# Kernel optimization log

Hardware: AMD Instinct MI355X
Metric: run time of the kernel (lower is better)

The kernel has to match this reference:

```python
import jax, jax.numpy as jnp
import numpy as np

V, E, H2, T = 50000, 256, 512, 16  # vocab, embed, hidden_dim, tagset
H = H2 // 2                        # per-direction hidden
START, STOP = 14, 15
NEG = -10000.0


def setup_inputs() -> dict:
    key = jax.random.key(0)
    ks = jax.random.split(key, 13)
    s = 0.08
    tokens = jax.random.randint(ks[0], (32, 512), 0, V)
    embed_table = jax.random.normal(ks[1], (V, E), jnp.float32)
    Wi_f = jax.random.normal(ks[2], (4 * H, E), jnp.float32) * s
    Wh_f = jax.random.normal(ks[3], (4 * H, H), jnp.float32) * s
    bi_f = jnp.zeros((4 * H,), jnp.float32)
    bh_f = jnp.zeros((4 * H,), jnp.float32)
    Wi_b = jax.random.normal(ks[4], (4 * H, E), jnp.float32) * s
    Wh_b = jax.random.normal(ks[5], (4 * H, H), jnp.float32) * s
    bi_b = jnp.zeros((4 * H,), jnp.float32)
    bh_b = jnp.zeros((4 * H,), jnp.float32)
    Wt = jax.random.normal(ks[6], (T, H2), jnp.float32) * s
    bt = jnp.zeros((T,), jnp.float32)
    trans = jax.random.normal(ks[7], (T, T), jnp.float32)
    trans = trans.at[START, :].set(NEG).at[:, STOP].set(NEG)
    return {"tokens": tokens, "embed_table": embed_table,
            "Wi_f": Wi_f, "Wh_f": Wh_f, "bi_f": bi_f, "bh_f": bh_f,
            "Wi_b": Wi_b, "Wh_b": Wh_b, "bi_b": bi_b, "bh_b": bh_b,
            "Wt": Wt, "bt": bt, "transitions": trans}


def _lstm_dir(x, Wi, Wh, bi, bh, reverse=False):
    # x: [S, B, E] -> h seq [S, B, H], PyTorch gate order i,f,g,o
    S, B, _ = x.shape
    xs = x[::-1] if reverse else x
    pre = jnp.einsum('sbe,ge->sbg', xs, Wi) + bi + bh  # precompute input GEMM

    def step(carry, z_t):
        h, c = carry
        z = z_t + h @ Wh.T  # [B, 4H]
        i, f, g, o = jnp.split(z, 4, axis=-1)
        c = jax.nn.sigmoid(f) * c + jax.nn.sigmoid(i) * jnp.tanh(g)
        h = jax.nn.sigmoid(o) * jnp.tanh(c)
        return (h, c), h

    h0 = jnp.zeros((B, H), x.dtype)
    _, hs = jax.lax.scan(step, (h0, h0), pre)
    return hs[::-1] if reverse else hs


def reference(tokens, embed_table, Wi_f, Wh_f, bi_f, bh_f,
              Wi_b, Wh_b, bi_b, bh_b, Wt, bt, transitions):
    x = embed_table[tokens]                # [B, S, E]
    x = jnp.transpose(x, (1, 0, 2))        # [S, B, E] seq-first like nn.LSTM
    hf = _lstm_dir(x, Wi_f, Wh_f, bi_f, bh_f, reverse=False)
    hb = _lstm_dir(x, Wi_b, Wh_b, bi_b, bh_b, reverse=True)
    feats = jnp.concatenate([hf, hb], axis=-1)           # [S, B, 2H]
    emissions = jnp.einsum('sbh,th->sbt', feats, Wt) + bt  # [S, B, T]

    B = tokens.shape[0]
    alpha0 = jnp.full((B, T), NEG, jnp.float32).at[:, START].set(0.0)

    def crf_step(alpha, emit_t):
        # alpha: [B, T_prev]; transitions[next, prev]; emit_t: [B, T_next]
        scores = alpha[:, None, :] + transitions[None, :, :] + emit_t[:, :, None]
        return jax.nn.logsumexp(scores, axis=2), None

    alpha, _ = jax.lax.scan(crf_step, alpha0, emissions)
    log_Z = jax.nn.logsumexp(alpha + transitions[STOP][None, :], axis=1)  # [B]
    return log_Z
```

## Files before the change

### kernel.cpp

```cpp
#include <hip/hip_runtime.h>
#include <hip/hip_bf16.h>
#include <stdint.h>

typedef __attribute__((ext_vector_type(4))) float f32x4;
typedef __attribute__((ext_vector_type(8))) short bf16x8;

#define WS_XBF   0u
#define WS_WIR   8388608u
#define WS_BIAS  9437184u
#define WS_PRE   9445376u
#define WS_HALL  76554240u
#define WS_CTL   93364224u
#define WS_EMIS  93368320u
#define WS_CHK   94416896u
#define WS_FLG   WS_CHK

__device__ __forceinline__ unsigned short f2bf(float x) {
    union { float f; unsigned int u; } v; v.f = x;
    return (unsigned short)((v.u + 0x7FFFu + ((v.u >> 16) & 1u)) >> 16);
}
__device__ __forceinline__ float bf2f(unsigned short b) {
    union { float f; unsigned int u; } v; v.u = ((unsigned int)b) << 16; return v.f;
}
__device__ __forceinline__ unsigned int pack2(float a, float b) {
    return (unsigned int)f2bf(a) | ((unsigned int)f2bf(b) << 16);
}
__device__ __forceinline__ float sigf(float x)  { return 1.0f / (1.0f + __expf(-x)); }
__device__ __forceinline__ float tanhf_(float x){ return 1.0f - 2.0f / (__expf(2.0f * x) + 1.0f); }

__device__ __forceinline__ void lds_barrier() {
    asm volatile("s_waitcnt lgkmcnt(0)" ::: "memory");
    __builtin_amdgcn_s_barrier();
    __builtin_amdgcn_sched_barrier(0);
}

__global__ __launch_bounds__(256) void k_prep(
    const int* __restrict__ tokens, const float* __restrict__ embed,
    const float* __restrict__ Wi_f, const float* __restrict__ Wi_b,
    const float* __restrict__ bi_f, const float* __restrict__ bh_f,
    const float* __restrict__ bi_b, const float* __restrict__ bh_b,
    char* __restrict__ ws)
{
    int blk = blockIdx.x, tid = threadIdx.x;
    unsigned short* xbf  = (unsigned short*)(ws + WS_XBF);
    unsigned short* wir  = (unsigned short*)(ws + WS_WIR);
    float* biasr         = (float*)(ws + WS_BIAS);
    if (blk < 2048) {
        int rr = tid >> 5, cc = tid & 31;
        int r = blk * 8 + rr;
        int s = r >> 5, b = r & 31;
        int tok = tokens[b * 512 + s];
        int k = cc * 8;
        const float* src = embed + (size_t)tok * 256 + k;
        float4 a = *(const float4*)src;
        float4 c = *(const float4*)(src + 4);
        uint4 o; o.x = pack2(a.x, a.y); o.y = pack2(a.z, a.w);
        o.z = pack2(c.x, c.y); o.w = pack2(c.z, c.w);
        *(uint4*)(xbf + (size_t)r * 256 + k) = o;
    } else if (blk < 2304) {
        int rr = tid >> 5, cc = tid & 31;
        int rowp = (blk - 2048) * 8 + rr;
        int dir = rowp >> 10, q = rowp & 1023;
        int j = q >> 8, rs = q & 255;
        int g = rs >> 6, hl = rs & 63;
        int srow = g * 256 + j * 64 + hl;
        const float* W = dir ? Wi_b : Wi_f;
        int k = cc * 8;
        const float* src = W + (size_t)srow * 256 + k;
        float4 a = *(const float4*)src;
        float4 c = *(const float4*)(src + 4);
        uint4 o; o.x = pack2(a.x, a.y); o.y = pack2(a.z, a.w);
        o.z = pack2(c.x, c.y); o.w = pack2(c.z, c.w);
        *(uint4*)(wir + (size_t)rowp * 256 + k) = o;
        if (cc == 0)
            biasr[rowp] = dir ? (bi_b[srow] + bh_b[srow]) : (bi_f[srow] + bh_f[srow]);
    } else {
        if (blk == 2304 && tid < 16)
            ((unsigned int*)(ws + WS_CTL))[tid] = 0u;
        if (blk == 2305) {
            unsigned int* flg = (unsigned int*)(ws + WS_FLG);
            for (int u = tid; u < 2 * 513 * 4 * 32; u += 256) flg[u] = 0u;
        }
        size_t g = (size_t)(blk - 2304) * 256 + tid;
        uint4* hall4 = (uint4*)(ws + WS_HALL);
        const unsigned int NF = 0xFFFFFFFFu;
        for (size_t u = g; u < 1050624u; u += 65536u) {
            size_t slot = (u >> 10) % 513u;
            uint4 val;
            if (slot == 0) { val.x = 0u; val.y = 0u; val.z = 0u; val.w = 0u; }
            else           { val.x = NF; val.y = NF; val.z = NF; val.w = NF; }
            hall4[u] = val;
        }
    }
}

__global__ __launch_bounds__(256) void k_pregemm(char* __restrict__ ws)
{
    __shared__ unsigned short Asb[128 * 136];
    __shared__ unsigned short Bsb[64 * 136];
    const unsigned short* xbf = (const unsigned short*)(ws + WS_XBF);
    const unsigned short* wir = (const unsigned short*)(ws + WS_WIR);
    const float* biasr        = (const float*)(ws + WS_BIAS);
    unsigned short* pre       = (unsigned short*)(ws + WS_PRE);
    int blk = blockIdx.x, tid = threadIdx.x;
    int mb = blk >> 5, nb = blk & 31;
    int Mbase = mb * 128, Nbase = nb * 64;
    int w = tid >> 6, l = tid & 63, col = l & 15, quad = l >> 4;
    f32x4 acc[4][2];
    #pragma unroll
    for (int a = 0; a < 4; ++a)
        #pragma unroll
        for (int b = 0; b < 2; ++b) acc[a][b] = (f32x4){0.f, 0.f, 0.f, 0.f};

    for (int kh = 0; kh < 2; ++kh) {
        __syncthreads();
        #pragma unroll
        for (int i = 0; i < 8; ++i) {
            int c = tid + i * 256;
            int row = c >> 4, c16 = c & 15;
            uint4 v = *(const uint4*)(xbf + ((size_t)(Mbase + row) * 256 + kh * 128 + c16 * 8));
            *(uint4*)(Asb + row * 136 + c16 * 8) = v;
        }
        #pragma unroll
        for (int i = 0; i < 4; ++i) {
            int c = tid + i * 256;
            int row = c >> 4, c16 = c & 15;
            uint4 v = *(const uint4*)(wir + ((size_t)(Nbase + row) * 256 + kh * 128 + c16 * 8));
            *(uint4*)(Bsb + row * 136 + c16 * 8) = v;
        }
        __syncthreads();
        int mhalf = w >> 1, nh = w & 1;
        #pragma unroll
        for (int kt = 0; kt < 4; ++kt) {
            bf16x8 bfr[2];
            #pragma unroll
            for (int nn = 0; nn < 2; ++nn)
                bfr[nn] = *(const bf16x8*)(Bsb + (16 * (nh * 2 + nn) + col) * 136 + kt * 32 + quad * 8);
            #pragma unroll
            for (int mm = 0; mm < 4; ++mm) {
                bf16x8 afr = *(const bf16x8*)(Asb + (16 * (mhalf * 4 + mm) + col) * 136 + kt * 32 + quad * 8);
                #pragma unroll
                for (int nn = 0; nn < 2; ++nn)
                    acc[mm][nn] = __builtin_amdgcn_mfma_f32_16x16x32_bf16(afr, bfr[nn], acc[mm][nn], 0, 0, 0);
            }
        }
    }
    #pragma unroll
    for (int mm = 0; mm < 4; ++mm) {
        int m_t = (w >> 1) * 4 + mm;
        int s = (Mbase >> 5) + (m_t >> 1);
        int bhalf = m_t & 1;
        #pragma unroll
        for (int nn = 0; nn < 2; ++nn) {
            int ncol = Nbase + 16 * ((w & 1) * 2 + nn) + col;
            int dir = ncol >> 10, j = (ncol >> 8) & 3, r = ncol & 255;
            int g = r >> 6, hl16 = (r >> 4) & 3;
            int tidp = (bhalf * 4 + hl16) * 64 + l;
            float bv = biasr[ncol];
            f32x4 a = acc[mm][nn];
            uint2 o;
            o.x = pack2(a[0] + bv, a[1] + bv);
            o.y = pack2(a[2] + bv, a[3] + bv);
            size_t off = (((size_t)(dir * 512 + s) * 4 + j) * 512 + tidp) * 16 + g * 4;
            *(uint2*)(pre + off) = o;
        }
    }
}

__global__ __launch_bounds__(512, 2) void k_rec(
    const float* __restrict__ Wh_f, const float* __restrict__ Wh_b, char* __restrict__ ws)
{
    __shared__ unsigned short hbuf[32 * 264];
    __shared__ char stpad[71680];
    __shared__ int sRole;
    __shared__ int goCnt;
    int tid = threadIdx.x;

    if (tid == 0) {
        ((volatile char*)stpad)[0] = 0;
        goCnt = 0;
        int xcd;
        asm volatile("s_getreg_b32 %0, hwreg(HW_REG_XCC_ID)" : "=s"(xcd));
        xcd &= 7;
        unsigned int* ctl = (unsigned int*)(ws + WS_CTL);
        unsigned int slot = __hip_atomic_fetch_add(&ctl[xcd], 1u,
                              __ATOMIC_RELAXED, __HIP_MEMORY_SCOPE_AGENT);
        int role = -1;
        if (slot < 8u) {
            if (slot == 7u) {
                unsigned int expv = 0u;
                __hip_atomic_compare_exchange_strong(&ctl[8], &expv, (unsigned int)(xcd + 1),
                    __ATOMIC_RELAXED, __ATOMIC_RELAXED, __HIP_MEMORY_SCOPE_AGENT);
            }
            unsigned int ts; long gc = 0;
            do {
                ts = __hip_atomic_fetch_add(&ctl[8], 0u,
                        __ATOMIC_RELAXED, __HIP_MEMORY_SCOPE_AGENT);
            } while (ts == 0u && ++gc < (1L << 26));
            if (ts == (unsigned int)(xcd + 1)) role = (int)slot;
        }
        sRole = role;
    }
    __syncthreads();
    int role = sRole;
    if (role < 0) return;
    int dir = role >> 2, j = role & 3;

    int w = tid >> 6, l = tid & 63, col = l & 15, quad = l >> 4;
    int m = w >> 2, hl16 = w & 3;
    const float* Wh = dir ? Wh_b : Wh_f;
    const unsigned short* pre = (const unsigned short*)(ws + WS_PRE);
    unsigned short* hall      = (unsigned short*)(ws + WS_HALL);
    unsigned int* flags       = (unsigned int*)(ws + WS_FLG);

    bf16x8 wf[4][8];
    #pragma unroll
    for (int g = 0; g < 4; ++g) {
        int grow = g * 256 + j * 64 + hl16 * 16 + col;
        #pragma unroll
        for (int kt = 0; kt < 8; ++kt) {
            const float* src = Wh + (size_t)grow * 256 + kt * 32 + quad * 8;
            float4 x0 = *(const float4*)src;
            float4 x1 = *(const float4*)(src + 4);
            bf16x8 f;
            f[0] = (short)f2bf(x0.x); f[1] = (short)f2bf(x0.y);
            f[2] = (short)f2bf(x0.z); f[3] = (short)f2bf(x0.w);
            f[4] = (short)f2bf(x1.x); f[5] = (short)f2bf(x1.y);
            f[6] = (short)f2bf(x1.z); f[7] = (short)f2bf(x1.w);
            wf[g][kt] = f;
        }
    }
    __syncthreads();

    float cst[4] = {0.f, 0.f, 0.f, 0.f};
    size_t hbase_u = (size_t)dir * 513 * 8192;
    int row0 = tid >> 6, c8 = tid & 63;
    int jr = (tid < 3) ? (tid + (tid >= j ? 1 : 0)) : -1;

    uint4 pn0, pn1;
    {
        int s0 = dir ? 511 : 0;
        const uint4* pp = (const uint4*)(pre + ((((size_t)(dir * 512 + s0)) * 4 + j) * 512 + tid) * 16);
        pn0 = pp[0]; pn1 = pp[1];
    }

    for (int st = 0; st < 512; ++st) {
        uint4 p0 = pn0, p1 = pn1;

        if (st > 0) {
            if (jr >= 0) {
                unsigned int* fl = flags + ((size_t)((dir * 513 + st) * 4 + jr)) * 32;
                int rnd = 0;
                for (;;) {
                    unsigned int expv = 0u;
                    __hip_atomic_compare_exchange_strong(fl, &expv, 0u,
                        __ATOMIC_RELAXED, __ATOMIC_RELAXED, __HIP_MEMORY_SCOPE_WORKGROUP);
                    if (expv != 0u) break;
                    if (++rnd > (1 << 18)) break;
                }
                __hip_atomic_fetch_add(&goCnt, 1, __ATOMIC_RELAXED, __HIP_MEMORY_SCOPE_WORKGROUP);
            }
            int target = 3 * st;
            long sg = 0;
            while (__hip_atomic_load(&goCnt, __ATOMIC_RELAXED, __HIP_MEMORY_SCOPE_WORKGROUP) < target) {
                if (++sg > (1L << 21)) break;
            }
            asm volatile("" ::: "memory");
        }

        const unsigned short* hsl = hall + hbase_u + (size_t)st * 8192;
        unsigned long long v[4];
        #pragma unroll
        for (int i = 0; i < 4; ++i)
            v[i] = *(const unsigned long long*)(hsl + (size_t)(tid + i * 512) * 4);
        #pragma unroll
        for (int i = 0; i < 4; ++i)
            *(unsigned long long*)(hbuf + (row0 + i * 8) * 264 + c8 * 4) = v[i];
        lds_barrier();

        f32x4 acc[4];
        #pragma unroll
        for (int g = 0; g < 4; ++g) acc[g] = (f32x4){0.f, 0.f, 0.f, 0.f};
        #pragma unroll
        for (int kt = 0; kt < 8; ++kt) {
            bf16x8 af = *(const bf16x8*)(hbuf + (m * 16 + col) * 264 + kt * 32 + quad * 8);
            #pragma unroll
            for (int g = 0; g < 4; ++g)
                acc[g] = __builtin_amdgcn_mfma_f32_16x16x32_bf16(af, wf[g][kt], acc[g], 0, 0, 0);
        }
        unsigned int pw[8] = {p0.x, p0.y, p0.z, p0.w, p1.x, p1.y, p1.z, p1.w};
        float z[4][4];
        #pragma unroll
        for (int g = 0; g < 4; ++g) {
            #pragma unroll
            for (int r2 = 0; r2 < 2; ++r2) {
                unsigned int u = pw[g * 2 + r2];
                z[g][r2 * 2]     = acc[g][r2 * 2]     + bf2f((unsigned short)(u & 0xffff));
                z[g][r2 * 2 + 1] = acc[g][r2 * 2 + 1] + bf2f((unsigned short)(u >> 16));
            }
        }
        unsigned short hb16[4];
        #pragma unroll
        for (int r = 0; r < 4; ++r) {
            float ci = sigf(z[1][r]) * cst[r] + sigf(z[0][r]) * tanhf_(z[2][r]);
            cst[r] = ci;
            hb16[r] = f2bf(sigf(z[3][r]) * tanhf_(ci));
        }
        size_t dstb = hbase_u + (size_t)(st + 1) * 8192
                    + (size_t)(m * 16 + quad * 4) * 256 + j * 64 + hl16 * 16 + col;
        #pragma unroll
        for (int r = 0; r < 4; ++r)
            *(hall + dstb + (size_t)r * 256) = hb16[r];
        asm volatile("s_waitcnt vmcnt(0)" ::: "memory");
        __builtin_amdgcn_s_barrier();
        __builtin_amdgcn_sched_barrier(0);
        if (tid == 0)
            (void)__hip_atomic_exchange(flags + ((size_t)((dir * 513 + st + 1) * 4 + j)) * 32, 1u,
                                        __ATOMIC_RELAXED, __HIP_MEMORY_SCOPE_WORKGROUP);
        {
            int stn = (st < 511) ? st + 1 : st;
            int sn = dir ? (511 - stn) : stn;
            const uint4* pp = (const uint4*)(pre + ((((size_t)(dir * 512 + sn)) * 4 + j) * 512 + tid) * 16);
            pn0 = pp[0]; pn1 = pp[1];
        }
    }
}

__global__ __launch_bounds__(256) void k_emis(
    const float* __restrict__ Wt, const float* __restrict__ bt, char* __restrict__ ws)
{
    __shared__ float WtL[16 * 528];
    __shared__ unsigned short hrow[16 * 536];
    __shared__ float btL[16];
    int blk = blockIdx.x, tid = threadIdx.x;
    int sbb = blk * 16;
    int s = sbb >> 5, bbase = sbb & 31;
    const unsigned short* hall = (const unsigned short*)(ws + WS_HALL);
    float* emis = (float*)(ws + WS_EMIS);
    #pragma unroll
    for (int i = 0; i < 8; ++i) {
        int c = tid + i * 256;
        int trow = c >> 7, c128 = c & 127;
        float4 v = *(const float4*)(Wt + (size_t)trow * 512 + c128 * 4);
        *(float4*)(WtL + trow * 528 + c128 * 4) = v;
    }
    #pragma unroll
    for (int i = 0; i < 4; ++i) {
        int c = tid + i * 256;
        int row = c >> 6, c6 = c & 63, half = c6 >> 5, c16 = c6 & 31;
        size_t base = half == 0 ? (size_t)(s + 1) * 8192 : ((size_t)513 + (512 - s)) * 8192;
        uint4 v = *(const uint4*)(hall + base + (size_t)(bbase + row) * 256 + c16 * 8);
        *(uint4*)(hrow + row * 536 + half * 256 + c16 * 8) = v;
    }
    if (tid < 16) btL[tid] = bt[tid];
    __syncthreads();
    int t = tid >> 4, i = tid & 15;
    float acc = btL[t];
    const float* wrow = WtL + t * 528;
    const unsigned short* hr = hrow + i * 536;
    #pragma unroll 8
    for (int k = 0; k < 512; k += 4) {
        uint2 hu = *(const uint2*)(hr + k);
        float4 wv = *(const float4*)(wrow + k);
        acc += bf2f((unsigned short)(hu.x & 0xffff)) * wv.x
             + bf2f((unsigned short)(hu.x >> 16))    * wv.y
             + bf2f((unsigned short)(hu.y & 0xffff)) * wv.z
             + bf2f((unsigned short)(hu.y >> 16))    * wv.w;
    }
    emis[((size_t)(bbase + i) * 512 + s) * 16 + t] = acc;
}

__global__ __launch_bounds__(256) void k_crfc(const float* __restrict__ trans, char* __restrict__ ws)
{
    __shared__ float trL[16 * 17];
    __shared__ float est[16 * 16];
    __shared__ float Pb[2][16 * 17];
    int blk = blockIdx.x, tid = threadIdx.x;
    int b = blk >> 5, c = blk & 31;
    int t = tid >> 4, p = tid & 15;
    const float* emis = (const float*)(ws + WS_EMIS);
    float* chk = (float*)(ws + WS_CHK);
    trL[t * 17 + p] = trans[t * 16 + p];
    est[t * 16 + p] = emis[((size_t)b * 512 + c * 16 + t) * 16 + p];
    __syncthreads();
    float tr[16];
    #pragma unroll
    for (int q = 0; q < 16; ++q) tr[q] = trL[t * 17 + q];
    float out = trL[t * 17 + p] + est[0 * 16 + t];
    Pb[0][t * 17 + p] = out;
    __syncthreads();
    int cur = 0;
    for (int si = 1; si < 16; ++si) {
        float v[16]; float mx = -3.0e38f;
        #pragma unroll
        for (int q = 0; q < 16; ++q) { v[q] = tr[q] + Pb[cur][q * 17 + p]; mx = fmaxf(mx, v[q]); }
        float ss = 0.f;
        #pragma unroll
        for (int q = 0; q < 16; ++q) ss += __expf(v[q] - mx);
        out = est[si * 16 + t] + mx + __logf(ss);
        Pb[1 - cur][t * 17 + p] = out;
        __syncthreads();
        cur = 1 - cur;
    }
    chk[(size_t)(b * 32 + c) * 256 + t * 16 + p] = out;
}

__global__ __launch_bounds__(256) void k_crff(
    const float* __restrict__ trans, char* __restrict__ ws, float* __restrict__ out)
{
    __shared__ float Cst[16 * 17];
    __shared__ float Pb[2][16 * 17];
    __shared__ float af[16];
    int b = blockIdx.x, tid = threadIdx.x;
    int t = tid >> 4, p = tid & 15;
    const float* chk = (const float*)(ws + WS_CHK);
    Pb[0][t * 17 + p] = chk[(size_t)(b * 32) * 256 + t * 16 + p];
    __syncthreads();
    int cur = 0;
    for (int ci = 1; ci < 32; ++ci) {
        Cst[t * 17 + p] = chk[(size_t)(b * 32 + ci) * 256 + t * 16 + p];
        __syncthreads();
        float v[16]; float mx = -3.0e38f;
        #pragma unroll
        for (int q = 0; q < 16; ++q) { v[q] = Cst[t * 17 + q] + Pb[cur][q * 17 + p]; mx = fmaxf(mx, v[q]); }
        float ss = 0.f;
        #pragma unroll
        for (int q = 0; q < 16; ++q) ss += __expf(v[q] - mx);
        float outv = mx + __logf(ss);
        Pb[1 - cur][t * 17 + p] = outv;
        __syncthreads();
        cur = 1 - cur;
    }
    float vfin = Pb[cur][t * 17 + p] + ((p == 14) ? 0.0f : -10000.0f);
    Cst[t * 17 + p] = vfin;
    __syncthreads();
    if (tid < 16) {
        float mx = -3.0e38f;
        for (int q = 0; q < 16; ++q) mx = fmaxf(mx, Cst[tid * 17 + q]);
        float ss = 0.f;
        for (int q = 0; q < 16; ++q) ss += __expf(Cst[tid * 17 + q] - mx);
        af[tid] = mx + __logf(ss) + trans[15 * 16 + tid];
    }
    __syncthreads();
    if (tid == 0) {
        float mx = -3.0e38f;
        for (int q = 0; q < 16; ++q) mx = fmaxf(mx, af[q]);
        float ss = 0.f;
        for (int q = 0; q < 16; ++q) ss += __expf(af[q] - mx);
        out[b] = mx + __logf(ss);
    }
}

extern "C" void kernel_launch(void* const* d_in, const int* in_sizes, int n_in,
                              void* d_out, int out_size, void* d_ws, size_t ws_size,
                              hipStream_t stream)
{
    const int*   tokens = (const int*)d_in[0];
    const float* embed  = (const float*)d_in[1];
    const float* Wi_f   = (const float*)d_in[2];
    const float* Wh_f   = (const float*)d_in[3];
    const float* bi_f   = (const float*)d_in[4];
    const float* bh_f   = (const float*)d_in[5];
    const float* Wi_b   = (const float*)d_in[6];
    const float* Wh_b   = (const float*)d_in[7];
    const float* bi_b   = (const float*)d_in[8];
    const float* bh_b   = (const float*)d_in[9];
    const float* Wt     = (const float*)d_in[10];
    const float* bt     = (const float*)d_in[11];
    const float* trans  = (const float*)d_in[12];
    char* ws = (char*)d_ws;
    float* out = (float*)d_out;

    hipLaunchKernelGGL(k_prep, dim3(2560), dim3(256), 0, stream,
                       tokens, embed, Wi_f, Wi_b, bi_f, bh_f, bi_b, bh_b, ws);
    hipLaunchKernelGGL(k_pregemm, dim3(4096), dim3(256), 0, stream, ws);
    hipLaunchKernelGGL(k_rec, dim3(128), dim3(512), 0, stream, Wh_f, Wh_b, ws);
    hipLaunchKernelGGL(k_emis, dim3(1024), dim3(256), 0, stream, Wt, bt, ws);
    hipLaunchKernelGGL(k_crfc, dim3(1024), dim3(256), 0, stream, trans, ws);
    hipLaunchKernelGGL(k_crff, dim3(32), dim3(256), 0, stream, trans, ws, out);
}
```

Measured before the change: 1.724 ms.

## Repartition LSTM recurrence by batch half and hidden half with local LDS reuse

The recurrent kernel changes from 4 blocks per direction each owning a 64-unit hidden slice over all 32 batch rows to 2x2 blocks per direction each owning 16 batch rows and 128 hidden units. Each block keeps its own half of h in double-buffered LDS and starts the MFMAs on that local half before waiting on the single peer's flag, then loads only the peer half from global memory. This cuts each step's wait from three producers to one and overlaps part of the recurrent GEMM with that wait. The hall layout, flag indexing, init and emission loader are reworked to match, and the spin timeouts are shortened, which could cause silent early exits if a peer stalls.

```diff
diff --git a/kernel.cpp b/kernel.cpp
--- a/kernel.cpp
+++ b/kernel.cpp
@@ -79,18 +79,13 @@
             ((unsigned int*)(ws + WS_CTL))[tid] = 0u;
         if (blk == 2305) {
             unsigned int* flg = (unsigned int*)(ws + WS_FLG);
-            for (int u = tid; u < 2 * 513 * 4 * 32; u += 256) flg[u] = 0u;
+            for (int u = tid; u < 4 * 513 * 2 * 32; u += 256) flg[u] = 0u;
         }
         size_t g = (size_t)(blk - 2304) * 256 + tid;
         uint4* hall4 = (uint4*)(ws + WS_HALL);
-        const unsigned int NF = 0xFFFFFFFFu;
-        for (size_t u = g; u < 1050624u; u += 65536u) {
-            size_t slot = (u >> 10) % 513u;
-            uint4 val;
-            if (slot == 0) { val.x = 0u; val.y = 0u; val.z = 0u; val.w = 0u; }
-            else           { val.x = NF; val.y = NF; val.z = NF; val.w = NF; }
-            hall4[u] = val;
-        }
+        uint4 z; z.x = 0u; z.y = 0u; z.z = 0u; z.w = 0u;
+        for (size_t u = g; u < 1050624u; u += 65536u)
+            hall4[u] = z;
     }
 }
 
@@ -170,15 +165,15 @@
 __global__ __launch_bounds__(512, 2) void k_rec(
     const float* __restrict__ Wh_f, const float* __restrict__ Wh_b, char* __restrict__ ws)
 {
-    __shared__ unsigned short hbuf[32 * 264];
+    __shared__ unsigned short hbuf[2 * 16 * 264];
     __shared__ char stpad[71680];
     __shared__ int sRole;
-    __shared__ int goCnt;
+    __shared__ int go;
     int tid = threadIdx.x;
 
     if (tid == 0) {
         ((volatile char*)stpad)[0] = 0;
-        goCnt = 0;
+        go = 0;
         int xcd;
         asm volatile("s_getreg_b32 %0, hwreg(HW_REG_XCC_ID)" : "=s"(xcd));
         xcd &= 7;
@@ -204,10 +199,9 @@
     __syncthreads();
     int role = sRole;
     if (role < 0) return;
-    int dir = role >> 2, j = role & 3;
+    int dir = role >> 2, b2 = (role >> 1) & 1, uh = role & 1;
 
     int w = tid >> 6, l = tid & 63, col = l & 15, quad = l >> 4;
-    int m = w >> 2, hl16 = w & 3;
     const float* Wh = dir ? Wh_b : Wh_f;
     const unsigned short* pre = (const unsigned short*)(ws + WS_PRE);
     unsigned short* hall      = (unsigned short*)(ws + WS_HALL);
@@ -216,7 +210,7 @@
     bf16x8 wf[4][8];
     #pragma unroll
     for (int g = 0; g < 4; ++g) {
-        int grow = g * 256 + j * 64 + hl16 * 16 + col;
+        int grow = g * 256 + uh * 128 + w * 16 + col;
         #pragma unroll
         for (int kt = 0; kt < 8; ++kt) {
             const float* src = Wh + (size_t)grow * 256 + kt * 32 + quad * 8;
@@ -230,64 +224,81 @@
             wf[g][kt] = f;
         }
     }
+    for (int u = tid; u < 4224; u += 512) ((unsigned int*)hbuf)[u] = 0;
     __syncthreads();
 
     float cst[4] = {0.f, 0.f, 0.f, 0.f};
-    size_t hbase_u = (size_t)dir * 513 * 8192;
-    int row0 = tid >> 6, c8 = tid & 63;
-    int jr = (tid < 3) ? (tid + (tid >= j ? 1 : 0)) : -1;
+    int jpre = uh * 2 + (w >> 2);
+    int tidp = (b2 * 4 + (w & 3)) * 64 + l;
+    size_t rb = (size_t)(dir * 2 + b2) * 513;
+    int rrow = l >> 2, cpart = l & 3;
 
     uint4 pn0, pn1;
     {
         int s0 = dir ? 511 : 0;
-        const uint4* pp = (const uint4*)(pre + ((((size_t)(dir * 512 + s0)) * 4 + j) * 512 + tid) * 16);
+        const uint4* pp = (const uint4*)(pre + ((((size_t)(dir * 512 + s0)) * 4 + jpre) * 512 + tidp) * 16);
         pn0 = pp[0]; pn1 = pp[1];
     }
 
     for (int st = 0; st < 512; ++st) {
+        int cur = st & 1;
+        unsigned short* hb_cur = hbuf + cur * 4224;
+        unsigned short* hb_nxt = hbuf + (cur ^ 1) * 4224;
         uint4 p0 = pn0, p1 = pn1;
+        {
+            int stn = (st < 511) ? st + 1 : st;
+            int sn = dir ? (511 - stn) : stn;
+            const uint4* pp = (const uint4*)(pre + ((((size_t)(dir * 512 + sn)) * 4 + jpre) * 512 + tidp) * 16);
+            pn0 = pp[0]; pn1 = pp[1];
+        }
+
+        f32x4 acc[4];
+        #pragma unroll
+        for (int g = 0; g < 4; ++g) acc[g] = (f32x4){0.f, 0.f, 0.f, 0.f};
+
+        #pragma unroll
+        for (int k2 = 0; k2 < 4; ++k2) {
+            int kt = uh * 4 + k2;
+            bf16x8 af = *(const bf16x8*)(hb_cur + col * 264 + kt * 32 + quad * 8);
+            #pragma unroll
+            for (int g = 0; g < 4; ++g)
+                acc[g] = __builtin_amdgcn_mfma_f32_16x16x32_bf16(af, wf[g][kt], acc[g], 0, 0, 0);
+        }
 
         if (st > 0) {
-            if (jr >= 0) {
-                unsigned int* fl = flags + ((size_t)((dir * 513 + st) * 4 + jr)) * 32;
+            if (tid == 0) {
+                unsigned int* fl = flags + ((rb + st) * 2 + (uh ^ 1)) * 32;
                 int rnd = 0;
                 for (;;) {
                     unsigned int expv = 0u;
                     __hip_atomic_compare_exchange_strong(fl, &expv, 0u,
                         __ATOMIC_RELAXED, __ATOMIC_RELAXED, __HIP_MEMORY_SCOPE_WORKGROUP);
                     if (expv != 0u) break;
-                    if (++rnd > (1 << 18)) break;
+                    if (++rnd > (1 << 16)) break;
                 }
-                __hip_atomic_fetch_add(&goCnt, 1, __ATOMIC_RELAXED, __HIP_MEMORY_SCOPE_WORKGROUP);
+                __hip_atomic_store(&go, st, __ATOMIC_RELAXED, __HIP_MEMORY_SCOPE_WORKGROUP);
             }
-            int target = 3 * st;
             long sg = 0;
-            while (__hip_atomic_load(&goCnt, __ATOMIC_RELAXED, __HIP_MEMORY_SCOPE_WORKGROUP) < target) {
-                if (++sg > (1L << 21)) break;
+            while (__hip_atomic_load(&go, __ATOMIC_RELAXED, __HIP_MEMORY_SCOPE_WORKGROUP) < st) {
+                if (++sg > (1L << 20)) break;
             }
             asm volatile("" ::: "memory");
-        }
-
-        const unsigned short* hsl = hall + hbase_u + (size_t)st * 8192;
-        unsigned long long v[4];
-        #pragma unroll
-        for (int i = 0; i < 4; ++i)
-            v[i] = *(const unsigned long long*)(hsl + (size_t)(tid + i * 512) * 4);
-        #pragma unroll
-        for (int i = 0; i < 4; ++i)
-            *(unsigned long long*)(hbuf + (row0 + i * 8) * 264 + c8 * 4) = v[i];
+            size_t srcb = (rb + st) * 4096 + (size_t)(uh ^ 1) * 2048 + (size_t)tid * 4;
+            unsigned long long pv = *(const unsigned long long*)(hall + srcb);
+            int prow = tid >> 5, ploc = (tid * 4) & 127;
+            *(unsigned long long*)(hb_cur + prow * 264 + (uh ^ 1) * 128 + ploc) = pv;
+        }
         lds_barrier();
 
-        f32x4 acc[4];
-        #pragma unroll
-        for (int g = 0; g < 4; ++g) acc[g] = (f32x4){0.f, 0.f, 0.f, 0.f};
-        #pragma unroll
-        for (int kt = 0; kt < 8; ++kt) {
-            bf16x8 af = *(const bf16x8*)(hbuf + (m * 16 + col) * 264 + kt * 32 + quad * 8);
+        #pragma unroll
+        for (int k2 = 0; k2 < 4; ++k2) {
+            int kt = (uh ^ 1) * 4 + k2;
+            bf16x8 af = *(const bf16x8*)(hb_cur + col * 264 + kt * 32 + quad * 8);
             #pragma unroll
             for (int g = 0; g < 4; ++g)
                 acc[g] = __builtin_amdgcn_mfma_f32_16x16x32_bf16(af, wf[g][kt], acc[g], 0, 0, 0);
         }
+
         unsigned int pw[8] = {p0.x, p0.y, p0.z, p0.w, p1.x, p1.y, p1.z, p1.w};
         float z[4][4];
         #pragma unroll
@@ -306,23 +317,21 @@
             cst[r] = ci;
             hb16[r] = f2bf(sigf(z[3][r]) * tanhf_(ci));
         }
-        size_t dstb = hbase_u + (size_t)(st + 1) * 8192
-                    + (size_t)(m * 16 + quad * 4) * 256 + j * 64 + hl16 * 16 + col;
         #pragma unroll
         for (int r = 0; r < 4; ++r)
-            *(hall + dstb + (size_t)r * 256) = hb16[r];
-        asm volatile("s_waitcnt vmcnt(0)" ::: "memory");
+            hb_nxt[(quad * 4 + r) * 264 + uh * 128 + w * 16 + col] = hb16[r];
+        asm volatile("s_waitcnt lgkmcnt(0)" ::: "memory");
+        __builtin_amdgcn_sched_barrier(0);
+        unsigned long long hv = *(const unsigned long long*)
+            (hb_nxt + rrow * 264 + uh * 128 + w * 16 + cpart * 4);
+        size_t pub = (rb + st + 1) * 4096 + (size_t)uh * 2048 + rrow * 128 + w * 16 + cpart * 4;
+        *(unsigned long long*)(hall + pub) = hv;
+        asm volatile("s_waitcnt vmcnt(0) lgkmcnt(0)" ::: "memory");
         __builtin_amdgcn_s_barrier();
         __builtin_amdgcn_sched_barrier(0);
         if (tid == 0)
-            (void)__hip_atomic_exchange(flags + ((size_t)((dir * 513 + st + 1) * 4 + j)) * 32, 1u,
+            (void)__hip_atomic_exchange(flags + ((rb + st + 1) * 2 + uh) * 32, 1u,
                                         __ATOMIC_RELAXED, __HIP_MEMORY_SCOPE_WORKGROUP);
-        {
-            int stn = (st < 511) ? st + 1 : st;
-            int sn = dir ? (511 - stn) : stn;
-            const uint4* pp = (const uint4*)(pre + ((((size_t)(dir * 512 + sn)) * 4 + j) * 512 + tid) * 16);
-            pn0 = pp[0]; pn1 = pp[1];
-        }
     }
 }
 
@@ -335,6 +344,7 @@
     int blk = blockIdx.x, tid = threadIdx.x;
     int sbb = blk * 16;
     int s = sbb >> 5, bbase = sbb & 31;
+    int b2 = bbase >> 4;
     const unsigned short* hall = (const unsigned short*)(ws + WS_HALL);
     float* emis = (float*)(ws + WS_EMIS);
     #pragma unroll
@@ -347,10 +357,13 @@
     #pragma unroll
     for (int i = 0; i < 4; ++i) {
         int c = tid + i * 256;
-        int row = c >> 6, c6 = c & 63, half = c6 >> 5, c16 = c6 & 31;
-        size_t base = half == 0 ? (size_t)(s + 1) * 8192 : ((size_t)513 + (512 - s)) * 8192;
-        uint4 v = *(const uint4*)(hall + base + (size_t)(bbase + row) * 256 + c16 * 8);
-        *(uint4*)(hrow + row * 536 + half * 256 + c16 * 8) = v;
+        int row = c >> 6, c6 = c & 63, dsel = c6 >> 5, c16 = c6 & 31;
+        int uh = (c16 >> 4) & 1, within = (c16 & 15) * 8;
+        size_t base = (dsel == 0)
+            ? ((size_t)(b2 * 513) + (size_t)(s + 1)) * 4096
+            : ((size_t)((2 + b2) * 513) + (size_t)(512 - s)) * 4096;
+        uint4 v = *(const uint4*)(hall + base + (size_t)uh * 2048 + row * 128 + within);
+        *(uint4*)(hrow + row * 536 + dsel * 256 + c16 * 8) = v;
     }
     if (tid < 16) btL[tid] = bt[tid];
     __syncthreads();
```

After: 4.631 ms. 169% more time.
